# Kernel optimization log

Hardware: AMD Instinct MI355X
Metric: run time of the kernel (lower is better)

The kernel has to match this reference:

```python
import jax, jax.numpy as jnp
import numpy as np

D = 512; N = 1536; H = 4; DH = D // H
MAX_INT = 5; BINS = 100; LAYERS = 3


def _mha(q_in, k_in, v_in, in_w, in_b, out_w, out_b):
    """PyTorch-style nn.MultiheadAttention (batch of 1). Returns (out [Nq,D], head-avg weights [Nq,Nk])."""
    wq, wk, wv = in_w[:D], in_w[D:2 * D], in_w[2 * D:]
    bq, bk, bv = in_b[:D], in_b[D:2 * D], in_b[2 * D:]
    n_q, n_k = q_in.shape[0], k_in.shape[0]
    q = (q_in @ wq.T + bq).reshape(n_q, H, DH).transpose(1, 0, 2)  # [H,Nq,dh]
    k = (k_in @ wk.T + bk).reshape(n_k, H, DH).transpose(1, 0, 2)
    v = (v_in @ wv.T + bv).reshape(n_k, H, DH).transpose(1, 0, 2)
    scores = jnp.einsum('hqd,hkd->hqk', q, k) / jnp.sqrt(jnp.asarray(DH, q.dtype))
    w = jax.nn.softmax(scores, axis=-1)  # [H,Nq,Nk]
    out = jnp.einsum('hqk,hkd->hqd', w, v).transpose(1, 0, 2).reshape(n_q, D)
    out = out @ out_w.T + out_b
    return out, w.mean(0)


def setup_inputs() -> dict:
    key = jax.random.key(0)
    ks = jax.random.split(key, 12)
    s = 0.02
    return {
        'node_embeddings': jax.random.normal(ks[0], (N, D), jnp.float32),
        'time_positions': jax.random.uniform(ks[1], (N, 1), jnp.float32) * 10.0,
        'batch_indices': jnp.zeros((N,), jnp.int32),
        'W_time': jax.random.normal(ks[2], (D, 1), jnp.float32) * s,
        'b_time': jnp.zeros((D,), jnp.float32),
        'in_w': jax.random.normal(ks[3], (3 * D, D), jnp.float32) * s,
        'in_b': jnp.zeros((3 * D,), jnp.float32),
        'out_w': jax.random.normal(ks[4], (D, D), jnp.float32) * s,
        'out_b': jnp.zeros((D,), jnp.float32),
        'ic_w1': jax.random.normal(ks[5], (128, D), jnp.float32) * s,
        'ic_b1': jnp.zeros((128,), jnp.float32),
        'ic_w2': jax.random.normal(ks[6], (MAX_INT, 128), jnp.float32) * s,
        'ic_b2': jnp.zeros((MAX_INT,), jnp.float32),
        'ref_w1': jax.random.normal(ks[7], (LAYERS, 128, D + 2), jnp.float32) * s,
        'ref_b1': jnp.zeros((LAYERS, 128), jnp.float32),
        'ref_w2': jax.random.normal(ks[8], (LAYERS, 2 * BINS, 128), jnp.float32) * s,
        'ref_b2': jnp.zeros((LAYERS, 2 * BINS), jnp.float32),
        'weight_params': jnp.linspace(-0.5, 0.5, BINS).astype(jnp.float32),
        'qp_w': jax.random.normal(ks[9], (D, D + 2), jnp.float32) * s,
        'qp_b': jnp.zeros((D,), jnp.float32),
    }


def _forward(node_embeddings, time_positions, W_time, b_time, in_w, in_b, out_w, out_b,
             ic_w1, ic_b1, ic_w2, ic_b2, ref_w1, ref_b1, ref_w2, ref_b2,
             weight_params, qp_w, qp_b):
    x = node_embeddings + time_positions @ W_time.T + b_time  # [N,D]
    attn_out, _ = _mha(x, x, x, in_w, in_b, out_w, out_b)      # [N,D]
    pooled = attn_out.mean(0)                                   # [D]
    probs = jax.nn.softmax(ic_w2 @ jax.nn.relu(ic_w1 @ pooled + ic_b1) + ic_b2)
    num_intervals = jnp.argmax(probs) + 1
    interval_mask = jnp.arange(MAX_INT) < num_intervals
    t_min, t_max = time_positions.min(), time_positions.max()
    grid = jnp.linspace(t_min, t_max, MAX_INT + 1)
    start, end = grid[:-1], grid[1:]                            # [MAX_INT]
    n = attn_out.shape[0]
    ones = jnp.ones((n, 1), attn_out.dtype)

    def per_interval(s_i, e_i, w1, b1, w2, b2):
        query = jnp.concatenate([attn_out, ones * s_i, ones * e_i], axis=-1)  # [N,D+2]
        qp = query @ qp_w.T + qp_b                                            # [N,D]
        h = jax.nn.relu(query @ w1.T + b1)
        logits = h @ w2.T + b2                                                # [N,2*BINS]
        s_off = (jax.nn.softmax(logits[:, :BINS], axis=-1) * weight_params).sum(-1)  # [N]
        e_off = (jax.nn.softmax(logits[:, BINS:], axis=-1) * weight_params).sum(-1)
        _, aw = _mha(qp, attn_out, attn_out, in_w, in_b, out_w, out_b)        # [N,N]
        return (aw * s_off).sum(), (aw * e_off).sum()

    for l in range(LAYERS):  # layers have distinct params; intervals are independent within a layer
        ds, de = jax.vmap(per_interval, in_axes=(0, 0, None, None, None, None))(
            start, end, ref_w1[l], ref_b1[l], ref_w2[l], ref_b2[l])
        start = start + ds
        end = end + de

    final_bounds = jnp.stack([start, end], axis=-1)  # [MAX_INT,2]
    return final_bounds, interval_mask


def reference(node_embeddings, time_positions, batch_indices, W_time, b_time, in_w, in_b,
              out_w, out_b, ic_w1, ic_b1, ic_w2, ic_b2, ref_w1, ref_b1, ref_w2, ref_b2,
              weight_params, qp_w, qp_b):
    return _forward(node_embeddings, time_positions, W_time, b_time, in_w, in_b, out_w, out_b,
                    ic_w1, ic_b1, ic_w2, ic_b2, ref_w1, ref_b1, ref_w2, ref_b2,
                    weight_params, qp_w, qp_b)
```

## Files before the change

kernel.cpp:

```cpp
#include <hip/hip_runtime.h>
#include <hip/hip_bf16.h>

typedef __hip_bfloat16 bf16;
typedef __bf16 bf16x8 __attribute__((ext_vector_type(8)));
typedef float f32x4 __attribute__((ext_vector_type(4)));

#define DD   512
#define NT   1536
#define NH   4
#define DHD  128
#define NBINS 100
#define MAXI 5
#define NL   3
#define RSQRT_DH 0.08838834764831845f

#define OFF_X      ((size_t)0)
#define OFF_QKV    (OFF_X    + (size_t)NT*DD)
#define OFF_ATT    (OFF_QKV  + (size_t)NT*3*DD)
#define OFF_CTX    (OFF_ATT  + (size_t)NT*DD)
#define OFF_K2     (OFF_CTX  + (size_t)NT*DD)
#define OFF_QP0    (OFF_K2   + (size_t)NT*DD)
#define OFF_Q0     (OFF_QP0  + (size_t)NT*DD)
#define OFF_H0     (OFF_Q0   + (size_t)NT*DD)
#define OFF_HR     (OFF_H0   + (size_t)NT*384)
#define OFF_LG     (OFF_HR   + (size_t)MAXI*NT*128)
#define OFF_AARR   (OFF_LG   + (size_t)MAXI*NT*200)
#define OFF_BARR   (OFF_AARR + (size_t)NH*NT)
#define OFF_AV     (OFF_BARR + (size_t)NH*NT)
#define OFF_BV     (OFF_AV   + (size_t)DD)
#define OFF_SOFF   (OFF_BV   + (size_t)DD)
#define OFF_EOFF   (OFF_SOFF + (size_t)MAXI*NT)
#define OFF_RST    (OFF_EOFF + (size_t)MAXI*NT)
#define OFF_POOL   (OFF_RST  + (size_t)NH*NT*2)
#define OFF_SCAL   (OFF_POOL + (size_t)DD)
#define OFF_S      (OFF_SCAL + (size_t)64)
#define SC_START 0
#define SC_END   5
#define SC_DSDE  10
#define SC_CNT   20
#define OFF_QPT  (OFF_QP0)
#define OFF_M2   (OFF_QP0 + (size_t)512*512)
#define OFF_B2   (OFF_QP0 + (size_t)2*512*512)
#define PSLICE   ((size_t)NH*NT*16)

__global__ void k_pre(const float* __restrict__ t, float* ws) {
    __shared__ float smn[256], smx[256];
    int tid = threadIdx.x;
    ws[OFF_POOL + tid] = 0.f; ws[OFF_POOL + 256 + tid] = 0.f;
    float mn = 1e30f, mx = -1e30f;
    for (int i = tid; i < NT; i += 256) { float v = t[i]; mn = fminf(mn, v); mx = fmaxf(mx, v); }
    smn[tid] = mn; smx[tid] = mx; __syncthreads();
    for (int s = 128; s; s >>= 1) {
        if (tid < s) { smn[tid] = fminf(smn[tid], smn[tid + s]); smx[tid] = fmaxf(smx[tid], smx[tid + s]); }
        __syncthreads();
    }
    if (tid == 0) {
        float tmin = smn[0], tmax = smx[0];
        for (int i = 0; i < MAXI; i++) {
            ws[OFF_SCAL + SC_START + i] = tmin + (tmax - tmin) * (float)i / 5.0f;
            ws[OFF_SCAL + SC_END + i]   = tmin + (tmax - tmin) * (float)(i + 1) / 5.0f;
        }
    }
}

__global__ void k_qpt(const float* __restrict__ qp_w, float* ws) {
    __shared__ float tb[32][33];
    int c0 = blockIdx.x * 32, d0 = blockIdx.y * 32;
    int tid = threadIdx.x;
    int dd = tid >> 5, cc = tid & 31;
#pragma unroll
    for (int p = 0; p < 4; p++)
        tb[dd + p * 8][cc] = qp_w[(size_t)(d0 + dd + p * 8) * 514 + c0 + cc];
    __syncthreads();
    int cc2 = tid >> 5, dd2 = tid & 31;
    float* qpT = ws + OFF_QPT;
#pragma unroll
    for (int p = 0; p < 4; p++)
        qpT[(size_t)(c0 + cc2 + p * 8) * 512 + d0 + dd2] = tb[dd2][cc2 + p * 8];
}

template <int BF16OUT>
__global__ __launch_bounds__(256) void k_mgemm(
    const float* __restrict__ A, int lda, long long aZ,
    const float* __restrict__ B, int ldb, long long bZ,
    void* __restrict__ Cv, int ldc, long long cZ,
    int N, int K, float alpha, const float* __restrict__ bias)
{
    int z = blockIdx.z;
    A += (size_t)z * aZ; B += (size_t)z * bZ;
    int m0 = blockIdx.y * 128, n0 = blockIdx.x * 128;
    __shared__ __bf16 As[128 * 40];
    __shared__ __bf16 Bs[128 * 40];
    int tid = threadIdx.x;
    int r = tid >> 1, hh = tid & 1;
    int w = tid >> 6, lane = tid & 63;
    int wm = (w & 1) * 64, wn = (w >> 1) * 64;
    int lr = lane & 15, lq = lane >> 4;
    f32x4 acc[4][4];
#pragma unroll
    for (int i = 0; i < 4; i++)
#pragma unroll
        for (int j = 0; j < 4; j++) acc[i][j] = (f32x4){0.f, 0.f, 0.f, 0.f};

    int gnr = n0 + r;
    const float* arow = A + (size_t)(m0 + r) * lda + hh * 16;
    const float* brow = B + (size_t)gnr * ldb + hh * 16;
    __bf16* awr = &As[r * 40 + hh * 16];
    __bf16* bwr = &Bs[r * 40 + hh * 16];

    for (int k0 = 0; k0 < K; k0 += 32) {
        __bf16 ta[16] __attribute__((aligned(16)));
        __bf16 tb[16] __attribute__((aligned(16)));
#pragma unroll
        for (int q = 0; q < 8; q++) {
            float2 f = *(const float2*)(arow + k0 + 2 * q);
            ta[2 * q] = (__bf16)f.x; ta[2 * q + 1] = (__bf16)f.y;
        }
        if (gnr < N) {
#pragma unroll
            for (int q = 0; q < 8; q++) {
                float2 f = *(const float2*)(brow + k0 + 2 * q);
                tb[2 * q] = (__bf16)f.x; tb[2 * q + 1] = (__bf16)f.y;
            }
        } else {
#pragma unroll
            for (int q = 0; q < 16; q++) tb[q] = (__bf16)0.f;
        }
        __syncthreads();
        *(bf16x8*)awr = *(bf16x8*)ta;
        *(bf16x8*)(awr + 8) = *(bf16x8*)(ta + 8);
        *(bf16x8*)bwr = *(bf16x8*)tb;
        *(bf16x8*)(bwr + 8) = *(bf16x8*)(tb + 8);
        __syncthreads();
        bf16x8 af[4], bfr[4];
#pragma unroll
        for (int i = 0; i < 4; i++) af[i] = *(bf16x8*)&As[(wm + i * 16 + lr) * 40 + lq * 8];
#pragma unroll
        for (int j = 0; j < 4; j++) bfr[j] = *(bf16x8*)&Bs[(wn + j * 16 + lr) * 40 + lq * 8];
#pragma unroll
        for (int i = 0; i < 4; i++)
#pragma unroll
            for (int j = 0; j < 4; j++)
                acc[i][j] = __builtin_amdgcn_mfma_f32_16x16x32_bf16(af[i], bfr[j], acc[i][j], 0, 0, 0);
    }
#pragma unroll
    for (int i = 0; i < 4; i++) {
#pragma unroll
        for (int r4 = 0; r4 < 4; r4++) {
            int gm = m0 + wm + i * 16 + lq * 4 + r4;
#pragma unroll
            for (int j = 0; j < 4; j++) {
                int gn = n0 + wn + j * 16 + lr;
                if (gn < N) {
                    float v = acc[i][j][r4] * alpha + (bias ? bias[gn] : 0.f);
                    if (BF16OUT) ((bf16*)Cv)[cZ * z + (size_t)gm * ldc + gn] = __float2bfloat16(v);
                    else         ((float*)Cv)[cZ * z + (size_t)gm * ldc + gn] = v;
                }
            }
        }
    }
}

template <int BF16OUT>
__global__ __launch_bounds__(256) void k_g64(
    const float* __restrict__ A, int lda, long long aZ,
    const float* __restrict__ B, int ldb, long long bZ,
    void* __restrict__ Cv, int ldc, long long cZ,
    int N, int K, float alpha, const float* __restrict__ bias)
{
    int z = blockIdx.z;
    A += (size_t)z * aZ; B += (size_t)z * bZ;
    int m0 = blockIdx.y * 64, n0 = blockIdx.x * 64;
    __shared__ __bf16 As[64 * 40];
    __shared__ __bf16 Bs[64 * 40];
    int tid = threadIdx.x;
    int r = tid >> 2, quad = tid & 3;
    int w = tid >> 6, lane = tid & 63;
    int wm = (w & 1) * 32, wn = (w >> 1) * 32;
    int lr = lane & 15, lq = lane >> 4;
    f32x4 acc[2][2];
#pragma unroll
    for (int i = 0; i < 2; i++)
#pragma unroll
        for (int j = 0; j < 2; j++) acc[i][j] = (f32x4){0.f, 0.f, 0.f, 0.f};

    int gnr = n0 + r;
    const float* arow = A + (size_t)(m0 + r) * lda + quad * 8;
    const float* brow = B + (size_t)gnr * ldb + quad * 8;
    __bf16* awr = &As[r * 40 + quad * 8];
    __bf16* bwr = &Bs[r * 40 + quad * 8];

    for (int k0 = 0; k0 < K; k0 += 32) {
        __bf16 ta[8] __attribute__((aligned(16)));
        __bf16 tb[8] __attribute__((aligned(16)));
#pragma unroll
        for (int q = 0; q < 4; q++) {
            float2 f = *(const float2*)(arow + k0 + 2 * q);
            ta[2 * q] = (__bf16)f.x; ta[2 * q + 1] = (__bf16)f.y;
        }
        if (gnr < N) {
#pragma unroll
            for (int q = 0; q < 4; q++) {
                float2 f = *(const float2*)(brow + k0 + 2 * q);
                tb[2 * q] = (__bf16)f.x; tb[2 * q + 1] = (__bf16)f.y;
            }
        } else {
#pragma unroll
            for (int q = 0; q < 8; q++) tb[q] = (__bf16)0.f;
        }
        __syncthreads();
        *(bf16x8*)awr = *(bf16x8*)ta;
        *(bf16x8*)bwr = *(bf16x8*)tb;
        __syncthreads();
        bf16x8 af[2], bfr[2];
#pragma unroll
        for (int i = 0; i < 2; i++) af[i] = *(bf16x8*)&As[(wm + i * 16 + lr) * 40 + lq * 8];
#pragma unroll
        for (int j = 0; j < 2; j++) bfr[j] = *(bf16x8*)&Bs[(wn + j * 16 + lr) * 40 + lq * 8];
#pragma unroll
        for (int i = 0; i < 2; i++)
#pragma unroll
            for (int j = 0; j < 2; j++)
                acc[i][j] = __builtin_amdgcn_mfma_f32_16x16x32_bf16(af[i], bfr[j], acc[i][j], 0, 0, 0);
    }
#pragma unroll
    for (int i = 0; i < 2; i++) {
#pragma unroll
        for (int r4 = 0; r4 < 4; r4++) {
            int gm = m0 + wm + i * 16 + lq * 4 + r4;
#pragma unroll
            for (int j = 0; j < 2; j++) {
                int gn = n0 + wn + j * 16 + lr;
                if (gn < N) {
                    float v = acc[i][j][r4] * alpha + (bias ? bias[gn] : 0.f);
                    if (BF16OUT) ((bf16*)Cv)[cZ * z + (size_t)gm * ldc + gn] = __float2bfloat16(v);
                    else         ((float*)Cv)[cZ * z + (size_t)gm * ldc + gn] = v;
                }
            }
        }
    }
}

__global__ __launch_bounds__(256) void k_qkv(
    const float* __restrict__ emb, const float* __restrict__ t,
    const float* __restrict__ wt, const float* __restrict__ bt,
    const float* __restrict__ in_w, const float* __restrict__ in_b, float* ws)
{
    int m0 = blockIdx.y * 64, n0 = blockIdx.x * 64;
    __shared__ __bf16 As[64 * 40];
    __shared__ __bf16 Bs[64 * 40];
    int tid = threadIdx.x;
    int r = tid >> 2, quad = tid & 3;
    int w = tid >> 6, lane = tid & 63;
    int wm = (w & 1) * 32, wn = (w >> 1) * 32;
    int lr = lane & 15, lq = lane >> 4;
    f32x4 acc[2][2];
#pragma unroll
    for (int i = 0; i < 2; i++)
#pragma unroll
        for (int j = 0; j < 2; j++) acc[i][j] = (f32x4){0.f, 0.f, 0.f, 0.f};

    float trow = t[m0 + r];
    const float* arow = emb + (size_t)(m0 + r) * DD + quad * 8;
    const float* brow = in_w + (size_t)(n0 + r) * DD + quad * 8;
    __bf16* awr = &As[r * 40 + quad * 8];
    __bf16* bwr = &Bs[r * 40 + quad * 8];

    for (int k0 = 0; k0 < DD; k0 += 32) {
        __bf16 ta[8] __attribute__((aligned(16)));
        __bf16 tb[8] __attribute__((aligned(16)));
#pragma unroll
        for (int q = 0; q < 4; q++) {
            float2 e = *(const float2*)(arow + k0 + 2 * q);
            float2 wv = *(const float2*)(wt + k0 + quad * 8 + 2 * q);
            float2 bv = *(const float2*)(bt + k0 + quad * 8 + 2 * q);
            ta[2 * q]     = (__bf16)(e.x + trow * wv.x + bv.x);
            ta[2 * q + 1] = (__bf16)(e.y + trow * wv.y + bv.y);
            float2 f = *(const float2*)(brow + k0 + 2 * q);
            tb[2 * q] = (__bf16)f.x; tb[2 * q + 1] = (__bf16)f.y;
        }
        __syncthreads();
        *(bf16x8*)awr = *(bf16x8*)ta;
        *(bf16x8*)bwr = *(bf16x8*)tb;
        __syncthreads();
        bf16x8 af[2], bfr[2];
#pragma unroll
        for (int i = 0; i < 2; i++) af[i] = *(bf16x8*)&As[(wm + i * 16 + lr) * 40 + lq * 8];
#pragma unroll
        for (int j = 0; j < 2; j++) bfr[j] = *(bf16x8*)&Bs[(wn + j * 16 + lr) * 40 + lq * 8];
#pragma unroll
        for (int i = 0; i < 2; i++)
#pragma unroll
            for (int j = 0; j < 2; j++)
                acc[i][j] = __builtin_amdgcn_mfma_f32_16x16x32_bf16(af[i], bfr[j], acc[i][j], 0, 0, 0);
    }
    float* qkv = ws + OFF_QKV;
    float* Vt  = ws + OFF_X;
#pragma unroll
    for (int i = 0; i < 2; i++)
#pragma unroll
        for (int j = 0; j < 2; j++) {
            int gn = n0 + wn + j * 16 + lr;
            int gmb = m0 + wm + i * 16 + lq * 4;
            float b = in_b[gn];
            f32x4 vv = acc[i][j];
            vv[0] += b; vv[1] += b; vv[2] += b; vv[3] += b;
            if (gn < 2 * DD) {
#pragma unroll
                for (int r4 = 0; r4 < 4; r4++)
                    qkv[(size_t)(gmb + r4) * (3 * DD) + gn] = vv[r4];
            } else {
                *(float4*)&Vt[(size_t)(gn - 2 * DD) * NT + gmb] = *(float4*)&vv;
            }
        }
}

__global__ __launch_bounds__(256) void k_oproj(
    const float* __restrict__ out_w, const float* __restrict__ out_b, float* ws)
{
    int m0 = blockIdx.y * 64, n0 = blockIdx.x * 64;
    __shared__ __bf16 As[64 * 40];
    __shared__ __bf16 Bs[64 * 40];
    __shared__ float ps[64];
    int tid = threadIdx.x;
    int r = tid >> 2, quad = tid & 3;
    int w = tid >> 6, lane = tid & 63;
    int wm = (w & 1) * 32, wn = (w >> 1) * 32;
    int lr = lane & 15, lq = lane >> 4;
    f32x4 acc[2][2];
#pragma unroll
    for (int i = 0; i < 2; i++)
#pragma unroll
        for (int j = 0; j < 2; j++) acc[i][j] = (f32x4){0.f, 0.f, 0.f, 0.f};
    if (tid < 64) ps[tid] = 0.f;

    const float* a0 = ws + OFF_CTX + (size_t)(m0 + r) * DD + quad * 8;
    const float* a1 = ws + OFF_HR  + (size_t)(m0 + r) * DD + quad * 8;
    const float* brow = out_w + (size_t)(n0 + r) * DD + quad * 8;
    __bf16* awr = &As[r * 40 + quad * 8];
    __bf16* bwr = &Bs[r * 40 + quad * 8];

    for (int k0 = 0; k0 < DD; k0 += 32) {
        __bf16 ta[8] __attribute__((aligned(16)));
        __bf16 tb[8] __attribute__((aligned(16)));
#pragma unroll
        for (int q = 0; q < 4; q++) {
            float2 x = *(const float2*)(a0 + k0 + 2 * q);
            float2 y = *(const float2*)(a1 + k0 + 2 * q);
            ta[2 * q]     = (__bf16)(x.x + y.x);
            ta[2 * q + 1] = (__bf16)(x.y + y.y);
            float2 f = *(const float2*)(brow + k0 + 2 * q);
            tb[2 * q] = (__bf16)f.x; tb[2 * q + 1] = (__bf16)f.y;
        }
        __syncthreads();
        *(bf16x8*)awr = *(bf16x8*)ta;
        *(bf16x8*)bwr = *(bf16x8*)tb;
        __syncthreads();
        bf16x8 af[2], bfr[2];
#pragma unroll
        for (int i = 0; i < 2; i++) af[i] = *(bf16x8*)&As[(wm + i * 16 + lr) * 40 + lq * 8];
#pragma unroll
        for (int j = 0; j < 2; j++) bfr[j] = *(bf16x8*)&Bs[(wn + j * 16 + lr) * 40 + lq * 8];
#pragma unroll
        for (int i = 0; i < 2; i++)
#pragma unroll
            for (int j = 0; j < 2; j++)
                acc[i][j] = __builtin_amdgcn_mfma_f32_16x16x32_bf16(af[i], bfr[j], acc[i][j], 0, 0, 0);
    }
    float* att = ws + OFF_ATT;
#pragma unroll
    for (int j = 0; j < 2; j++) {
        int gn = n0 + wn + j * 16 + lr;
        float b = out_b[gn];
        float colsum = 0.f;
#pragma unroll
        for (int i = 0; i < 2; i++)
#pragma unroll
            for (int r4 = 0; r4 < 4; r4++) {
                int gm = m0 + wm + i * 16 + lq * 4 + r4;
                float v = acc[i][j][r4] + b;
                att[(size_t)gm * DD + gn] = v;
                colsum += v;
            }
        atomicAdd(&ps[wn + j * 16 + lr], colsum);
    }
    __syncthreads();
    if (tid < 64) atomicAdd(&ws[OFF_POOL + n0 + tid], ps[tid]);
}

__global__ __launch_bounds__(256) void k_trip(
    const float* __restrict__ in_w, const float* __restrict__ in_b,
    const float* __restrict__ ref_w1, const float* __restrict__ ref_b1, float* ws)
{
    int bx = blockIdx.x;
    const float* B; const float* bias; float* C; int ldb, ldc, n0;
    if (bx < 8)       { B = in_w + (size_t)DD * DD; ldb = DD;  bias = in_b + DD;   C = ws + OFF_K2; ldc = DD;  n0 = bx * 64; }
    else if (bx < 16) { B = ws + OFF_M2;            ldb = 512; bias = ws + OFF_B2; C = ws + OFF_Q0; ldc = DD;  n0 = (bx - 8) * 64; }
    else              { B = ref_w1;                 ldb = 514; bias = ref_b1;      C = ws + OFF_H0; ldc = 384; n0 = (bx - 16) * 64; }
    const float* A = ws + OFF_ATT;
    int m0 = blockIdx.y * 64;
    __shared__ __bf16 As[64 * 40];
    __shared__ __bf16 Bs[64 * 40];
    int tid = threadIdx.x;
    int r = tid >> 2, quad = tid & 3;
    int w = tid >> 6, lane = tid & 63;
    int wm = (w & 1) * 32, wn = (w >> 1) * 32;
    int lr = lane & 15, lq = lane >> 4;
    f32x4 acc[2][2];
#pragma unroll
    for (int i = 0; i < 2; i++)
#pragma unroll
        for (int j = 0; j < 2; j++) acc[i][j] = (f32x4){0.f, 0.f, 0.f, 0.f};

    const float* arow = A + (size_t)(m0 + r) * DD + quad * 8;
    const float* brow = B + (size_t)(n0 + r) * ldb + quad * 8;
    __bf16* awr = &As[r * 40 + quad * 8];
    __bf16* bwr = &Bs[r * 40 + quad * 8];

    for (int k0 = 0; k0 < DD; k0 += 32) {
        __bf16 ta[8] __attribute__((aligned(16)));
        __bf16 tb[8] __attribute__((aligned(16)));
#pragma unroll
        for (int q = 0; q < 4; q++) {
            float2 f = *(const float2*)(arow + k0 + 2 * q);
            ta[2 * q] = (__bf16)f.x; ta[2 * q + 1] = (__bf16)f.y;
            float2 g = *(const float2*)(brow + k0 + 2 * q);
            tb[2 * q] = (__bf16)g.x; tb[2 * q + 1] = (__bf16)g.y;
        }
        __syncthreads();
        *(bf16x8*)awr = *(bf16x8*)ta;
        *(bf16x8*)bwr = *(bf16x8*)tb;
        __syncthreads();
        bf16x8 af[2], bfr[2];
#pragma unroll
        for (int i = 0; i < 2; i++) af[i] = *(bf16x8*)&As[(wm + i * 16 + lr) * 40 + lq * 8];
#pragma unroll
        for (int j = 0; j < 2; j++) bfr[j] = *(bf16x8*)&Bs[(wn + j * 16 + lr) * 40 + lq * 8];
#pragma unroll
        for (int i = 0; i < 2; i++)
#pragma unroll
            for (int j = 0; j < 2; j++)
                acc[i][j] = __builtin_amdgcn_mfma_f32_16x16x32_bf16(af[i], bfr[j], acc[i][j], 0, 0, 0);
    }
#pragma unroll
    for (int i = 0; i < 2; i++)
#pragma unroll
        for (int r4 = 0; r4 < 4; r4++) {
            int gm = m0 + wm + i * 16 + lq * 4 + r4;
#pragma unroll
            for (int j = 0; j < 2; j++) {
                int gn = n0 + wn + j * 16 + lr;
                C[(size_t)gm * ldc + gn] = acc[i][j][r4] + bias[gn];
            }
        }
}

__global__ __launch_bounds__(256) void k_rstats(const bf16* __restrict__ S, float* ws) {
    int wave = threadIdx.x >> 6, lane = threadIdx.x & 63;
    int row = blockIdx.x * 4 + wave;
    const bf16* p = S + (size_t)row * NT;
    float v[24], m = -1e30f;
#pragma unroll
    for (int t = 0; t < 24; t++) { v[t] = __bfloat162float(p[t * 64 + lane]); m = fmaxf(m, v[t]); }
    for (int off = 32; off; off >>= 1) m = fmaxf(m, __shfl_xor(m, off));
    float s = 0.f;
#pragma unroll
    for (int t = 0; t < 24; t++) s += __expf(v[t] - m);
    for (int off = 32; off; off >>= 1) s += __shfl_xor(s, off);
    if (lane == 0) { ws[OFF_RST + 2 * row] = m; ws[OFF_RST + 2 * row + 1] = 1.f / s; }
}

__global__ __launch_bounds__(256) void k_rse(float* ws) {
    bf16* S = (bf16*)(ws + OFF_S);
    int wave = threadIdx.x >> 6, lane = threadIdx.x & 63;
    int row = blockIdx.x * 4 + wave;
    unsigned short* p = (unsigned short*)(S + (size_t)row * NT);
    union { uint4 u; unsigned short s[8]; } b[3];
    float v[24], m = -1e30f;
#pragma unroll
    for (int c = 0; c < 3; c++) {
        b[c].u = *(const uint4*)(p + c * 512 + lane * 8);
#pragma unroll
        for (int q = 0; q < 8; q++) {
            v[c * 8 + q] = __uint_as_float((unsigned)b[c].s[q] << 16);
            m = fmaxf(m, v[c * 8 + q]);
        }
    }
    for (int off = 32; off; off >>= 1) m = fmaxf(m, __shfl_xor(m, off));
#pragma unroll
    for (int c = 0; c < 3; c++) {
#pragma unroll
        for (int q = 0; q < 8; q++) {
            bf16 ov = __float2bfloat16(__expf(v[c * 8 + q] - m));
            b[c].s[q] = *(unsigned short*)&ov;
        }
        *(uint4*)(p + c * 512 + lane * 8) = b[c].u;
    }
}

__global__ __launch_bounds__(256) void k_pv(const bf16* __restrict__ S, float* ws) {
    int h = blockIdx.z;
    int m0 = blockIdx.y * 64;
    int n0 = (blockIdx.x & 1) * 64;
    int ks = blockIdx.x >> 1;
    const int KCH = NT / 2;
    int kbeg = ks * KCH;
    __shared__ __bf16 As[64 * 40];
    __shared__ __bf16 Bs[64 * 40];
    int tid = threadIdx.x;
    int r = tid >> 2, quad = tid & 3;
    int w = tid >> 6, lane = tid & 63;
    int wm = (w & 1) * 32, wn = (w >> 1) * 32;
    int lr = lane & 15, lq = lane >> 4;
    const float* rst = ws + OFF_RST;
    const float* Vt = ws + OFF_X + (size_t)h * DHD * NT;
    const bf16* Sh = S + (size_t)h * NT * NT;
    int row = m0 + r;
    float mrow = rst[2 * (h * NT + row)];
    const unsigned short* srow = (const unsigned short*)(Sh + (size_t)row * NT) + quad * 8;
    const float* brow = Vt + (size_t)(n0 + r) * NT + quad * 8;
    __bf16* awr = &As[r * 40 + quad * 8];
    __bf16* bwr = &Bs[r * 40 + quad * 8];
    f32x4 acc[2][2];
#pragma unroll
    for (int i = 0; i < 2; i++)
#pragma unroll
        for (int j = 0; j < 2; j++) acc[i][j] = (f32x4){0.f, 0.f, 0.f, 0.f};

    for (int k0 = kbeg; k0 < kbeg + KCH; k0 += 32) {
        union { uint4 u; unsigned short s[8]; } bb;
        bb.u = *(const uint4*)(srow + k0);
        __bf16 ta[8] __attribute__((aligned(16)));
        __bf16 tb[8] __attribute__((aligned(16)));
#pragma unroll
        for (int q = 0; q < 8; q++)
            ta[q] = (__bf16)__expf(__uint_as_float((unsigned)bb.s[q] << 16) - mrow);
#pragma unroll
        for (int q = 0; q < 4; q++) {
            float2 f = *(const float2*)(brow + k0 + 2 * q);
            tb[2 * q] = (__bf16)f.x; tb[2 * q + 1] = (__bf16)f.y;
        }
        __syncthreads();
        *(bf16x8*)awr = *(bf16x8*)ta;
        *(bf16x8*)bwr = *(bf16x8*)tb;
        __syncthreads();
        bf16x8 af[2], bfr[2];
#pragma unroll
        for (int i = 0; i < 2; i++) af[i] = *(bf16x8*)&As[(wm + i * 16 + lr) * 40 + lq * 8];
#pragma unroll
        for (int j = 0; j < 2; j++) bfr[j] = *(bf16x8*)&Bs[(wn + j * 16 + lr) * 40 + lq * 8];
#pragma unroll
        for (int i = 0; i < 2; i++)
#pragma unroll
            for (int j = 0; j < 2; j++)
                acc[i][j] = __builtin_amdgcn_mfma_f32_16x16x32_bf16(af[i], bfr[j], acc[i][j], 0, 0, 0);
    }
    float* dst = ws + (ks == 0 ? OFF_CTX : OFF_HR);
#pragma unroll
    for (int i = 0; i < 2; i++)
#pragma unroll
        for (int r4 = 0; r4 < 4; r4++) {
            int gm = m0 + wm + i * 16 + lq * 4 + r4;
            float ri = rst[2 * (h * NT + gm) + 1];
#pragma unroll
            for (int j = 0; j < 2; j++) {
                int gn = n0 + wn + j * 16 + lr;
                dst[(size_t)gm * DD + h * DHD + gn] = acc[i][j][r4] * ri;
            }
        }
}

__global__ void k_head(const float* __restrict__ icw1, const float* __restrict__ icb1,
                       const float* __restrict__ icw2, const float* __restrict__ icb2,
                       float* ws, float* out) {
    __shared__ float h1[128];
    __shared__ float lg[MAXI];
    int tid = threadIdx.x;
    float a = 0.f;
    for (int c = 0; c < DD; c++) a += icw1[(size_t)tid * DD + c] * ws[OFF_POOL + c];
    h1[tid] = fmaxf(a * (1.0f / NT) + icb1[tid], 0.f);
    __syncthreads();
    if (tid < MAXI) {
        float s = icb2[tid];
        for (int j = 0; j < 128; j++) s += icw2[tid * 128 + j] * h1[j];
        lg[tid] = s;
    }
    __syncthreads();
    if (tid == 0) {
        int best = 0; float bv = lg[0];
        for (int m = 1; m < MAXI; m++) if (lg[m] > bv) { bv = lg[m]; best = m; }
        int ni = best + 1;
        for (int i = 0; i < MAXI; i++) out[10 + i] = (i < ni) ? 1.f : 0.f;
    }
}

__global__ void k_uv(const float* __restrict__ in_w, const float* __restrict__ qp_w,
                     const float* __restrict__ qp_b, const float* __restrict__ in_b, float* ws) {
    __shared__ float su[DD], sv[DD], sb[DD];
    int tid = threadIdx.x;
    for (int c = tid; c < DD; c += 256) {
        su[c] = qp_w[c * 514 + 512]; sv[c] = qp_w[c * 514 + 513]; sb[c] = qp_b[c];
    }
    __syncthreads();
    int j = blockIdx.x * 256 + tid;
    float a = 0.f, b = 0.f, c2 = 0.f;
    for (int c = 0; c < DD; c++) {
        float w = in_w[(size_t)j * DD + c];
        a += w * su[c]; b += w * sv[c]; c2 += w * sb[c];
    }
    ws[OFF_AV + j] = a; ws[OFF_BV + j] = b; ws[OFF_B2 + j] = c2 + in_b[j];
}

__global__ __launch_bounds__(256) void k_ab(float* ws) {
    int wave = threadIdx.x >> 6, lane = threadIdx.x & 63;
    int row = blockIdx.x * 4 + wave;
    int h = row / NT, n = row % NT;
    const float* k2 = ws + OFF_K2 + (size_t)n * DD + h * DHD;
    const float* av = ws + OFF_AV + h * DHD;
    const float* bv = ws + OFF_BV + h * DHD;
    int d = lane * 2;
    float a = av[d] * k2[d] + av[d + 1] * k2[d + 1];
    float b = bv[d] * k2[d] + bv[d + 1] * k2[d + 1];
    for (int off = 32; off; off >>= 1) { a += __shfl_xor(a, off); b += __shfl_xor(b, off); }
    if (lane == 0) { ws[OFF_AARR + row] = a * RSQRT_DH; ws[OFF_BARR + row] = b * RSQRT_DH; }
}

__global__ __launch_bounds__(256) void k_lgs(
    const float* __restrict__ rw1, const float* __restrict__ rw2,
    const float* __restrict__ rb2, const float* __restrict__ wp, int l, float* ws)
{
    __shared__ float dsh[128];
    __shared__ __bf16 As[64 * 136];
    __shared__ __bf16 Bs[64 * 136];
    __shared__ __bf16 Ls[64 * 208];
    int tid = threadIdx.x;
    int m0 = blockIdx.x * 64;
    int i_int = m0 / NT;
    int nbase = m0 % NT;
    if (blockIdx.x == 0 && tid < 11) ws[OFF_SCAL + SC_DSDE + tid] = 0.f;
    if (tid < 128) {
        float s_i = ws[OFF_SCAL + SC_START + i_int], e_i = ws[OFF_SCAL + SC_END + i_int];
        const float* wr = rw1 + (size_t)(l * 128 + tid) * 514;
        dsh[tid] = s_i * wr[512] + e_i * wr[513];
    }
    __syncthreads();
    int r = tid >> 2, quad = tid & 3;
    {
        const float* arow = ws + OFF_H0 + (size_t)(nbase + r) * 384 + l * 128 + quad * 32;
        __bf16 tmp[32] __attribute__((aligned(16)));
#pragma unroll
        for (int q = 0; q < 16; q++) {
            float2 f = *(const float2*)(arow + 2 * q);
            int jj = quad * 32 + 2 * q;
            tmp[2 * q]     = (__bf16)fmaxf(f.x + dsh[jj], 0.f);
            tmp[2 * q + 1] = (__bf16)fmaxf(f.y + dsh[jj + 1], 0.f);
        }
        __bf16* aw = &As[r * 136 + quad * 32];
#pragma unroll
        for (int q = 0; q < 4; q++) *(bf16x8*)(aw + q * 8) = *(bf16x8*)(tmp + q * 8);
    }
    int w = tid >> 6, lane = tid & 63;
    int wm = (w & 1) * 32, wn = (w >> 1) * 32;
    int lr = lane & 15, lq = lane >> 4;
    for (int nt = 0; nt < 4; nt++) {
        int n0 = nt * 64;
        int gnr = n0 + r;
        __bf16 tmp[32] __attribute__((aligned(16)));
        if (gnr < 200) {
            const float* brow = rw2 + (size_t)gnr * 128 + quad * 32;
#pragma unroll
            for (int q = 0; q < 16; q++) {
                float2 f = *(const float2*)(brow + 2 * q);
                tmp[2 * q] = (__bf16)f.x; tmp[2 * q + 1] = (__bf16)f.y;
            }
        } else {
#pragma unroll
            for (int q = 0; q < 32; q++) tmp[q] = (__bf16)0.f;
        }
        __syncthreads();
        {
            __bf16* bw = &Bs[r * 136 + quad * 32];
#pragma unroll
            for (int q = 0; q < 4; q++) *(bf16x8*)(bw + q * 8) = *(bf16x8*)(tmp + q * 8);
        }
        __syncthreads();
        f32x4 acc[2][2];
#pragma unroll
        for (int i = 0; i < 2; i++)
#pragma unroll
            for (int j = 0; j < 2; j++) acc[i][j] = (f32x4){0.f, 0.f, 0.f, 0.f};
#pragma unroll
        for (int kk = 0; kk < 4; kk++) {
            bf16x8 af[2], bfr[2];
#pragma unroll
            for (int i = 0; i < 2; i++) af[i] = *(bf16x8*)&As[(wm + i * 16 + lr) * 136 + kk * 32 + lq * 8];
#pragma unroll
            for (int j = 0; j < 2; j++) bfr[j] = *(bf16x8*)&Bs[(wn + j * 16 + lr) * 136 + kk * 32 + lq * 8];
#pragma unroll
            for (int i = 0; i < 2; i++)
#pragma unroll
                for (int j = 0; j < 2; j++)
                    acc[i][j] = __builtin_amdgcn_mfma_f32_16x16x32_bf16(af[i], bfr[j], acc[i][j], 0, 0, 0);
        }
#pragma unroll
        for (int i = 0; i < 2; i++)
#pragma unroll
            for (int r4 = 0; r4 < 4; r4++) {
                int rl = wm + i * 16 + lq * 4 + r4;
#pragma unroll
                for (int j = 0; j < 2; j++) {
                    int gn = n0 + wn + j * 16 + lr;
                    if (gn < 200) Ls[rl * 208 + gn] = (__bf16)(acc[i][j][r4] + rb2[gn]);
                }
            }
    }
    __syncthreads();
    {
        int rloc = tid >> 2, q = tid & 3;
        int c0 = q * 50;
        const unsigned short* lrow = (const unsigned short*)&Ls[rloc * 208];
        float m = -1e30f;
#pragma unroll
        for (int c = 0; c < 50; c++)
            m = fmaxf(m, __uint_as_float((unsigned)lrow[c0 + c] << 16));
        m = fmaxf(m, __shfl_xor(m, 1));
        float den = 0.f, num = 0.f;
#pragma unroll
        for (int c = 0; c < 50; c++) {
            float p = __expf(__uint_as_float((unsigned)lrow[c0 + c] << 16) - m);
            den += p;
            int wc = c0 + c; if (wc >= NBINS) wc -= NBINS;
            num += p * wp[wc];
        }
        den += __shfl_xor(den, 1);
        num += __shfl_xor(num, 1);
        int n = nbase + rloc;
        if (q == 0)      ws[OFF_SOFF + (size_t)i_int * NT + n] = num / den;
        else if (q == 2) ws[OFF_EOFF + (size_t)i_int * NT + n] = num / den;
    }
}

__global__ __launch_bounds__(256) void k_eg(const bf16* __restrict__ E0, float* ws) {
    int h = blockIdx.z;
    int m0 = blockIdx.y * 128;
    int ks = blockIdx.x;
    const int KCH = NT / 8;
    __shared__ __bf16 As[128 * 40];
    __shared__ __bf16 Bs[16 * 40];
    int tid = threadIdx.x;
    int w = tid >> 6, lane = tid & 63;
    int lr = lane & 15, lq = lane >> 4;
    int r = tid >> 1, half = tid & 1;
    const bf16* Sh = E0 + (size_t)h * NT * NT;
    const unsigned short* arow = (const unsigned short*)(Sh + (size_t)(m0 + r) * NT) + half * 16;
    int wm = w * 32;
    f32x4 acc[2];
    acc[0] = (f32x4){0.f, 0.f, 0.f, 0.f};
    acc[1] = (f32x4){0.f, 0.f, 0.f, 0.f};
    int bc = tid >> 3, bk = tid & 7;
    int valid = (tid < 128) && (bc < 15);
    int ii = bc / 3, tt = bc - ii * 3;
    if (ii > 4) ii = 4;
    float s_i = 0.f, e_i = 0.f;
    if (valid) { s_i = ws[OFF_SCAL + SC_START + ii]; e_i = ws[OFF_SCAL + SC_END + ii]; }
    const float* Ar = ws + OFF_AARR + h * NT;
    const float* Br = ws + OFF_BARR + h * NT;
    const float* fo = ws + (tt == 2 ? OFF_EOFF : OFF_SOFF) + (size_t)ii * NT;

    for (int k0 = ks * KCH; k0 < ks * KCH + KCH; k0 += 32) {
        uint4 a0 = *(const uint4*)(arow + k0);
        uint4 a1 = *(const uint4*)(arow + k0 + 8);
        float bv[4] = {0.f, 0.f, 0.f, 0.f};
        if (valid) {
            float4 a4 = *(const float4*)(Ar + k0 + bk * 4);
            float4 b4 = *(const float4*)(Br + k0 + bk * 4);
            bv[0] = __expf(s_i * a4.x + e_i * b4.x);
            bv[1] = __expf(s_i * a4.y + e_i * b4.y);
            bv[2] = __expf(s_i * a4.z + e_i * b4.z);
            bv[3] = __expf(s_i * a4.w + e_i * b4.w);
            if (tt) {
                float4 f4 = *(const float4*)(fo + k0 + bk * 4);
                bv[0] *= f4.x; bv[1] *= f4.y; bv[2] *= f4.z; bv[3] *= f4.w;
            }
        }
        __syncthreads();
        *(uint4*)&As[r * 40 + half * 16] = a0;
        *(uint4*)&As[r * 40 + half * 16 + 8] = a1;
        if (tid < 128) {
            __bf16* bw = &Bs[bc * 40 + bk * 4];
            bw[0] = (__bf16)bv[0]; bw[1] = (__bf16)bv[1]; bw[2] = (__bf16)bv[2]; bw[3] = (__bf16)bv[3];
        }
        __syncthreads();
        bf16x8 bf0 = *(bf16x8*)&Bs[lr * 40 + lq * 8];
        bf16x8 af0 = *(bf16x8*)&As[(wm + lr) * 40 + lq * 8];
        bf16x8 af1 = *(bf16x8*)&As[(wm + 16 + lr) * 40 + lq * 8];
        acc[0] = __builtin_amdgcn_mfma_f32_16x16x32_bf16(af0, bf0, acc[0], 0, 0, 0);
        acc[1] = __builtin_amdgcn_mfma_f32_16x16x32_bf16(af1, bf0, acc[1], 0, 0, 0);
    }
    float* P = ws + OFF_LG + (size_t)ks * PSLICE;
    if (lr < 15) {
#pragma unroll
        for (int i = 0; i < 2; i++)
#pragma unroll
            for (int r4 = 0; r4 < 4; r4++) {
                int gm = m0 + wm + i * 16 + lq * 4 + r4;
                P[(size_t)(h * NT + gm) * 16 + lr] = acc[i][r4];
            }
    }
}

__global__ __launch_bounds__(256) void k_fin(float* ws) {
    __shared__ float part[4][10];
    int tid = threadIdx.x;
    int w = tid >> 6, lane = tid & 63;
    int row = blockIdx.x * 256 + tid;
    float acc[15];
#pragma unroll
    for (int c = 0; c < 15; c++) acc[c] = 0.f;
    for (int ks = 0; ks < 8; ks++) {
        const float* Pr = ws + OFF_LG + (size_t)ks * PSLICE + (size_t)row * 16;
#pragma unroll
        for (int c = 0; c < 15; c++) acc[c] += Pr[c];
    }
    float loc[10];
#pragma unroll
    for (int i = 0; i < MAXI; i++) {
        float den = acc[i * 3];
        loc[i]        = acc[i * 3 + 1] / den;
        loc[MAXI + i] = acc[i * 3 + 2] / den;
    }
#pragma unroll
    for (int c = 0; c < 10; c++)
        for (int off = 32; off; off >>= 1) loc[c] += __shfl_xor(loc[c], off);
    if (lane == 0) {
#pragma unroll
        for (int c = 0; c < 10; c++) part[w][c] = loc[c];
    }
    __syncthreads();
    if (tid < 10) {
        float s = part[0][tid] + part[1][tid] + part[2][tid] + part[3][tid];
        atomicAdd(&ws[OFF_SCAL + SC_DSDE + tid], s);
    }
    __threadfence();
    __syncthreads();
    if (tid == 0) {
        unsigned old = atomicAdd((unsigned*)&ws[OFF_SCAL + SC_CNT], 1u);
        if (old == 23) {
            for (int i = 0; i < MAXI; i++) {
                float ds = atomicAdd(&ws[OFF_SCAL + SC_DSDE + i], 0.f);
                float de = atomicAdd(&ws[OFF_SCAL + SC_DSDE + MAXI + i], 0.f);
                ws[OFF_SCAL + SC_START + i] += ds * 0.25f;
                ws[OFF_SCAL + SC_END + i]   += de * 0.25f;
            }
        }
    }
}

__global__ void k_final(const float* __restrict__ ws, float* out) {
    int tid = threadIdx.x;
    if (tid < MAXI) {
        out[2 * tid]     = ws[OFF_SCAL + SC_START + tid];
        out[2 * tid + 1] = ws[OFF_SCAL + SC_END + tid];
    }
}

extern "C" void kernel_launch(void* const* d_in, const int* in_sizes, int n_in,
                              void* d_out, int out_size, void* d_ws, size_t ws_size,
                              hipStream_t stream) {
    const float* emb    = (const float*)d_in[0];
    const float* tpos   = (const float*)d_in[1];
    const float* W_time = (const float*)d_in[3];
    const float* b_time = (const float*)d_in[4];
    const float* in_w   = (const float*)d_in[5];
    const float* in_b   = (const float*)d_in[6];
    const float* out_w  = (const float*)d_in[7];
    const float* out_b  = (const float*)d_in[8];
    const float* ic_w1  = (const float*)d_in[9];
    const float* ic_b1  = (const float*)d_in[10];
    const float* ic_w2  = (const float*)d_in[11];
    const float* ic_b2  = (const float*)d_in[12];
    const float* ref_w1 = (const float*)d_in[13];
    const float* ref_b1 = (const float*)d_in[14];
    const float* ref_w2 = (const float*)d_in[15];
    const float* ref_b2 = (const float*)d_in[16];
    const float* wp     = (const float*)d_in[17];
    const float* qp_w   = (const float*)d_in[18];
    const float* qp_b   = (const float*)d_in[19];
    float* ws  = (float*)d_ws;
    float* out = (float*)d_out;
    bf16* S = (bf16*)(ws + OFF_S);

    k_pre<<<1, 256, 0, stream>>>(tpos, ws);
    k_qpt<<<dim3(16, 16), 256, 0, stream>>>(qp_w, ws);
    k_g64<0><<<dim3(8, 8, 1), 256, 0, stream>>>(
        in_w, DD, 0, ws + OFF_QPT, 512, 0, ws + OFF_M2, 512, 0, 512, DD, 1.f, nullptr);
    k_uv<<<2, 256, 0, stream>>>(in_w, qp_w, qp_b, in_b, ws);

    k_qkv<<<dim3(24, 24), 256, 0, stream>>>(emb, tpos, W_time, b_time, in_w, in_b, ws);
    k_mgemm<1><<<dim3(12, 12, NH), 256, 0, stream>>>(
        ws + OFF_QKV, 3 * DD, DHD, ws + OFF_QKV + DD, 3 * DD, DHD,
        S, NT, (long long)NT * NT, NT, DHD, RSQRT_DH, nullptr);
    k_rstats<<<NH * NT / 4, 256, 0, stream>>>(S, ws);
    k_pv<<<dim3(4, NT / 64, NH), 256, 0, stream>>>(S, ws);
    k_oproj<<<dim3(8, 24), 256, 0, stream>>>(out_w, out_b, ws);
    k_head<<<1, 128, 0, stream>>>(ic_w1, ic_b1, ic_w2, ic_b2, ws, out);

    k_trip<<<dim3(22, 24), 256, 0, stream>>>(in_w, in_b, ref_w1, ref_b1, ws);
    k_ab<<<NH * NT / 4, 256, 0, stream>>>(ws);

    k_mgemm<1><<<dim3(12, 12, NH), 256, 0, stream>>>(
        ws + OFF_Q0, DD, DHD, ws + OFF_K2, DD, DHD,
        S, NT, (long long)NT * NT, NT, DHD, RSQRT_DH, nullptr);
    k_rse<<<NH * NT / 4, 256, 0, stream>>>(ws);

    for (int l = 0; l < NL; l++) {
        k_lgs<<<120, 256, 0, stream>>>(ref_w1, ref_w2 + (size_t)l * 200 * 128,
                                       ref_b2 + l * 200, wp, l, ws);
        k_eg<<<dim3(8, NT / 128, NH), 256, 0, stream>>>(S, ws);
        k_fin<<<NH * NT / 256, 256, 0, stream>>>(ws);
    }
    k_final<<<1, 32, 0, stream>>>(ws, out);
}
```

Baseline: 367.3 us.

## Fuse softmax row stats into score GEMM and merge small prep kernels

The score GEMM now emits per-tile row max and sum-of-exp partials, so the separate row-stats and row-stat-exp passes over the NxN score matrix are gone. The PV and evidence kernels recompute exp on the fly from the stored raw scores. Small setup kernels (min/max, transpose, qp GEMM, uv dot products) are merged into one multi-role launch, and the head and final-output kernels are folded into others. Launch count and full passes over the score matrix go down, in exchange for extra exp work inside the GEMM consumers.

```diff
diff --git a/kernel.cpp b/kernel.cpp
--- a/kernel.cpp
+++ b/kernel.cpp
@@ -38,59 +38,127 @@
 #define SC_END   5
 #define SC_DSDE  10
 #define SC_CNT   20
-#define OFF_QPT  (OFF_QP0)
 #define OFF_M2   (OFF_QP0 + (size_t)512*512)
 #define OFF_B2   (OFF_QP0 + (size_t)2*512*512)
 #define PSLICE   ((size_t)NH*NT*16)
-
-__global__ void k_pre(const float* __restrict__ t, float* ws) {
+#define OFF_STAT (OFF_LG + (size_t)8*PSLICE)
+
+__global__ __launch_bounds__(256) void k_misc(
+    const float* __restrict__ tpos, const float* __restrict__ in_w,
+    const float* __restrict__ in_b, const float* __restrict__ qp_w,
+    const float* __restrict__ qp_b, float* ws)
+{
+    __shared__ __bf16 As[64 * 40];
+    __shared__ __bf16 Bs[64 * 40];
     __shared__ float smn[256], smx[256];
-    int tid = threadIdx.x;
-    ws[OFF_POOL + tid] = 0.f; ws[OFF_POOL + 256 + tid] = 0.f;
-    float mn = 1e30f, mx = -1e30f;
-    for (int i = tid; i < NT; i += 256) { float v = t[i]; mn = fminf(mn, v); mx = fmaxf(mx, v); }
-    smn[tid] = mn; smx[tid] = mx; __syncthreads();
-    for (int s = 128; s; s >>= 1) {
-        if (tid < s) { smn[tid] = fminf(smn[tid], smn[tid + s]); smx[tid] = fmaxf(smx[tid], smx[tid + s]); }
-        __syncthreads();
-    }
-    if (tid == 0) {
-        float tmin = smn[0], tmax = smx[0];
-        for (int i = 0; i < MAXI; i++) {
-            ws[OFF_SCAL + SC_START + i] = tmin + (tmax - tmin) * (float)i / 5.0f;
-            ws[OFF_SCAL + SC_END + i]   = tmin + (tmax - tmin) * (float)(i + 1) / 5.0f;
-        }
-    }
-}
-
-__global__ void k_qpt(const float* __restrict__ qp_w, float* ws) {
-    __shared__ float tb[32][33];
-    int c0 = blockIdx.x * 32, d0 = blockIdx.y * 32;
-    int tid = threadIdx.x;
-    int dd = tid >> 5, cc = tid & 31;
-#pragma unroll
-    for (int p = 0; p < 4; p++)
-        tb[dd + p * 8][cc] = qp_w[(size_t)(d0 + dd + p * 8) * 514 + c0 + cc];
-    __syncthreads();
-    int cc2 = tid >> 5, dd2 = tid & 31;
-    float* qpT = ws + OFF_QPT;
-#pragma unroll
-    for (int p = 0; p < 4; p++)
-        qpT[(size_t)(c0 + cc2 + p * 8) * 512 + d0 + dd2] = tb[dd2][cc2 + p * 8];
-}
-
-template <int BF16OUT>
-__global__ __launch_bounds__(256) void k_mgemm(
+    int bx = blockIdx.x, tid = threadIdx.x;
+    if (bx < 64) {
+        int m0 = (bx >> 3) * 64, n0 = (bx & 7) * 64;
+        int r = tid >> 2, quad = tid & 3;
+        int w = tid >> 6, lane = tid & 63;
+        int wm = (w & 1) * 32, wn = (w >> 1) * 32;
+        int lr = lane & 15, lq = lane >> 4;
+        f32x4 acc[2][2];
+#pragma unroll
+        for (int i = 0; i < 2; i++)
+#pragma unroll
+            for (int j = 0; j < 2; j++) acc[i][j] = (f32x4){0.f, 0.f, 0.f, 0.f};
+        const float* arow = in_w + (size_t)(m0 + r) * DD + quad * 8;
+        int kk = tid >> 3, g = tid & 7;
+        for (int k0 = 0; k0 < DD; k0 += 32) {
+            __bf16 ta[8] __attribute__((aligned(16)));
+#pragma unroll
+            for (int q = 0; q < 4; q++) {
+                float2 f = *(const float2*)(arow + k0 + 2 * q);
+                ta[2 * q] = (__bf16)f.x; ta[2 * q + 1] = (__bf16)f.y;
+            }
+            const float* bsrc = qp_w + (size_t)(k0 + kk) * 514 + n0 + g * 8;
+            float4 b0 = *(const float4*)bsrc;
+            float4 b1 = *(const float4*)(bsrc + 4);
+            float bb[8] = {b0.x, b0.y, b0.z, b0.w, b1.x, b1.y, b1.z, b1.w};
+            __syncthreads();
+            *(bf16x8*)&As[r * 40 + quad * 8] = *(bf16x8*)ta;
+#pragma unroll
+            for (int q = 0; q < 8; q++) Bs[(g * 8 + q) * 40 + kk] = (__bf16)bb[q];
+            __syncthreads();
+            bf16x8 af[2], bfr[2];
+#pragma unroll
+            for (int i = 0; i < 2; i++) af[i] = *(bf16x8*)&As[(wm + i * 16 + lr) * 40 + lq * 8];
+#pragma unroll
+            for (int j = 0; j < 2; j++) bfr[j] = *(bf16x8*)&Bs[(wn + j * 16 + lr) * 40 + lq * 8];
+#pragma unroll
+            for (int i = 0; i < 2; i++)
+#pragma unroll
+                for (int j = 0; j < 2; j++)
+                    acc[i][j] = __builtin_amdgcn_mfma_f32_16x16x32_bf16(af[i], bfr[j], acc[i][j], 0, 0, 0);
+        }
+        float* M2 = ws + OFF_M2;
+#pragma unroll
+        for (int i = 0; i < 2; i++)
+#pragma unroll
+            for (int r4 = 0; r4 < 4; r4++) {
+                int gm = m0 + wm + i * 16 + lq * 4 + r4;
+#pragma unroll
+                for (int j = 0; j < 2; j++)
+                    M2[(size_t)gm * 512 + n0 + wn + j * 16 + lr] = acc[i][j][r4];
+            }
+    } else if (bx < 72) {
+        int w = tid >> 6, lane = tid & 63;
+        float su8[8], sv8[8], sb8[8];
+#pragma unroll
+        for (int q = 0; q < 8; q++) {
+            int c = lane * 8 + q;
+            su8[q] = qp_w[(size_t)c * 514 + 512];
+            sv8[q] = qp_w[(size_t)c * 514 + 513];
+            sb8[q] = qp_b[c];
+        }
+        int base = (bx - 64) * 64 + w * 16;
+        for (int t = 0; t < 16; t++) {
+            int row = base + t;
+            const float* wr = in_w + (size_t)row * DD + lane * 8;
+            float4 x0 = *(const float4*)wr, x1 = *(const float4*)(wr + 4);
+            float xa[8] = {x0.x, x0.y, x0.z, x0.w, x1.x, x1.y, x1.z, x1.w};
+            float a = 0.f, b = 0.f, c2 = 0.f;
+#pragma unroll
+            for (int q = 0; q < 8; q++) { a += xa[q] * su8[q]; b += xa[q] * sv8[q]; c2 += xa[q] * sb8[q]; }
+            for (int off = 32; off; off >>= 1) {
+                a += __shfl_xor(a, off); b += __shfl_xor(b, off); c2 += __shfl_xor(c2, off);
+            }
+            if (lane == 0) {
+                ws[OFF_AV + row] = a; ws[OFF_BV + row] = b; ws[OFF_B2 + row] = c2 + in_b[row];
+            }
+        }
+    } else {
+        ws[OFF_POOL + tid] = 0.f; ws[OFF_POOL + 256 + tid] = 0.f;
+        float mn = 1e30f, mx = -1e30f;
+        for (int i = tid; i < NT; i += 256) { float v = tpos[i]; mn = fminf(mn, v); mx = fmaxf(mx, v); }
+        smn[tid] = mn; smx[tid] = mx; __syncthreads();
+        for (int s = 128; s; s >>= 1) {
+            if (tid < s) { smn[tid] = fminf(smn[tid], smn[tid + s]); smx[tid] = fmaxf(smx[tid], smx[tid + s]); }
+            __syncthreads();
+        }
+        if (tid == 0) {
+            float tmin = smn[0], tmax = smx[0];
+            for (int i = 0; i < MAXI; i++) {
+                ws[OFF_SCAL + SC_START + i] = tmin + (tmax - tmin) * (float)i / 5.0f;
+                ws[OFF_SCAL + SC_END + i]   = tmin + (tmax - tmin) * (float)(i + 1) / 5.0f;
+            }
+        }
+    }
+}
+
+__global__ __launch_bounds__(256) void k_score(
     const float* __restrict__ A, int lda, long long aZ,
     const float* __restrict__ B, int ldb, long long bZ,
-    void* __restrict__ Cv, int ldc, long long cZ,
-    int N, int K, float alpha, const float* __restrict__ bias)
+    bf16* __restrict__ C, float* __restrict__ stat)
 {
     int z = blockIdx.z;
     A += (size_t)z * aZ; B += (size_t)z * bZ;
     int m0 = blockIdx.y * 128, n0 = blockIdx.x * 128;
     __shared__ __bf16 As[128 * 40];
     __shared__ __bf16 Bs[128 * 40];
+    __shared__ float sMax[4][64];
+    __shared__ float sSum[4][64];
     int tid = threadIdx.x;
     int r = tid >> 1, hh = tid & 1;
     int w = tid >> 6, lane = tid & 63;
@@ -102,29 +170,20 @@
 #pragma unroll
         for (int j = 0; j < 4; j++) acc[i][j] = (f32x4){0.f, 0.f, 0.f, 0.f};
 
-    int gnr = n0 + r;
     const float* arow = A + (size_t)(m0 + r) * lda + hh * 16;
-    const float* brow = B + (size_t)gnr * ldb + hh * 16;
+    const float* brow = B + (size_t)(n0 + r) * ldb + hh * 16;
     __bf16* awr = &As[r * 40 + hh * 16];
     __bf16* bwr = &Bs[r * 40 + hh * 16];
 
-    for (int k0 = 0; k0 < K; k0 += 32) {
+    for (int k0 = 0; k0 < DHD; k0 += 32) {
         __bf16 ta[16] __attribute__((aligned(16)));
         __bf16 tb[16] __attribute__((aligned(16)));
 #pragma unroll
         for (int q = 0; q < 8; q++) {
             float2 f = *(const float2*)(arow + k0 + 2 * q);
             ta[2 * q] = (__bf16)f.x; ta[2 * q + 1] = (__bf16)f.y;
-        }
-        if (gnr < N) {
-#pragma unroll
-            for (int q = 0; q < 8; q++) {
-                float2 f = *(const float2*)(brow + k0 + 2 * q);
-                tb[2 * q] = (__bf16)f.x; tb[2 * q + 1] = (__bf16)f.y;
-            }
-        } else {
-#pragma unroll
-            for (int q = 0; q < 16; q++) tb[q] = (__bf16)0.f;
+            float2 g = *(const float2*)(brow + k0 + 2 * q);
+            tb[2 * q] = (__bf16)g.x; tb[2 * q + 1] = (__bf16)g.y;
         }
         __syncthreads();
         *(bf16x8*)awr = *(bf16x8*)ta;
@@ -144,100 +203,47 @@
                 acc[i][j] = __builtin_amdgcn_mfma_f32_16x16x32_bf16(af[i], bfr[j], acc[i][j], 0, 0, 0);
     }
 #pragma unroll
-    for (int i = 0; i < 4; i++) {
+    for (int i = 0; i < 4; i++)
 #pragma unroll
         for (int r4 = 0; r4 < 4; r4++) {
             int gm = m0 + wm + i * 16 + lq * 4 + r4;
 #pragma unroll
             for (int j = 0; j < 4; j++) {
                 int gn = n0 + wn + j * 16 + lr;
-                if (gn < N) {
-                    float v = acc[i][j][r4] * alpha + (bias ? bias[gn] : 0.f);
-                    if (BF16OUT) ((bf16*)Cv)[cZ * z + (size_t)gm * ldc + gn] = __float2bfloat16(v);
-                    else         ((float*)Cv)[cZ * z + (size_t)gm * ldc + gn] = v;
-                }
-            }
-        }
-    }
-}
-
-template <int BF16OUT>
-__global__ __launch_bounds__(256) void k_g64(
-    const float* __restrict__ A, int lda, long long aZ,
-    const float* __restrict__ B, int ldb, long long bZ,
-    void* __restrict__ Cv, int ldc, long long cZ,
-    int N, int K, float alpha, const float* __restrict__ bias)
-{
-    int z = blockIdx.z;
-    A += (size_t)z * aZ; B += (size_t)z * bZ;
-    int m0 = blockIdx.y * 64, n0 = blockIdx.x * 64;
-    __shared__ __bf16 As[64 * 40];
-    __shared__ __bf16 Bs[64 * 40];
-    int tid = threadIdx.x;
-    int r = tid >> 2, quad = tid & 3;
-    int w = tid >> 6, lane = tid & 63;
-    int wm = (w & 1) * 32, wn = (w >> 1) * 32;
-    int lr = lane & 15, lq = lane >> 4;
-    f32x4 acc[2][2];
-#pragma unroll
-    for (int i = 0; i < 2; i++)
-#pragma unroll
-        for (int j = 0; j < 2; j++) acc[i][j] = (f32x4){0.f, 0.f, 0.f, 0.f};
-
-    int gnr = n0 + r;
-    const float* arow = A + (size_t)(m0 + r) * lda + quad * 8;
-    const float* brow = B + (size_t)gnr * ldb + quad * 8;
-    __bf16* awr = &As[r * 40 + quad * 8];
-    __bf16* bwr = &Bs[r * 40 + quad * 8];
-
-    for (int k0 = 0; k0 < K; k0 += 32) {
-        __bf16 ta[8] __attribute__((aligned(16)));
-        __bf16 tb[8] __attribute__((aligned(16)));
-#pragma unroll
-        for (int q = 0; q < 4; q++) {
-            float2 f = *(const float2*)(arow + k0 + 2 * q);
-            ta[2 * q] = (__bf16)f.x; ta[2 * q + 1] = (__bf16)f.y;
-        }
-        if (gnr < N) {
-#pragma unroll
-            for (int q = 0; q < 4; q++) {
-                float2 f = *(const float2*)(brow + k0 + 2 * q);
-                tb[2 * q] = (__bf16)f.x; tb[2 * q + 1] = (__bf16)f.y;
-            }
-        } else {
-#pragma unroll
-            for (int q = 0; q < 8; q++) tb[q] = (__bf16)0.f;
-        }
-        __syncthreads();
-        *(bf16x8*)awr = *(bf16x8*)ta;
-        *(bf16x8*)bwr = *(bf16x8*)tb;
-        __syncthreads();
-        bf16x8 af[2], bfr[2];
-#pragma unroll
-        for (int i = 0; i < 2; i++) af[i] = *(bf16x8*)&As[(wm + i * 16 + lr) * 40 + lq * 8];
-#pragma unroll
-        for (int j = 0; j < 2; j++) bfr[j] = *(bf16x8*)&Bs[(wn + j * 16 + lr) * 40 + lq * 8];
-#pragma unroll
-        for (int i = 0; i < 2; i++)
-#pragma unroll
-            for (int j = 0; j < 2; j++)
-                acc[i][j] = __builtin_amdgcn_mfma_f32_16x16x32_bf16(af[i], bfr[j], acc[i][j], 0, 0, 0);
-    }
-#pragma unroll
-    for (int i = 0; i < 2; i++) {
+                C[(size_t)z * NT * NT + (size_t)gm * NT + gn] =
+                    __float2bfloat16(acc[i][j][r4] * RSQRT_DH);
+            }
+        }
+#pragma unroll
+    for (int i = 0; i < 4; i++)
 #pragma unroll
         for (int r4 = 0; r4 < 4; r4++) {
-            int gm = m0 + wm + i * 16 + lq * 4 + r4;
-#pragma unroll
-            for (int j = 0; j < 2; j++) {
-                int gn = n0 + wn + j * 16 + lr;
-                if (gn < N) {
-                    float v = acc[i][j][r4] * alpha + (bias ? bias[gn] : 0.f);
-                    if (BF16OUT) ((bf16*)Cv)[cZ * z + (size_t)gm * ldc + gn] = __float2bfloat16(v);
-                    else         ((float*)Cv)[cZ * z + (size_t)gm * ldc + gn] = v;
-                }
-            }
-        }
+            float m = -1e30f;
+#pragma unroll
+            for (int j = 0; j < 4; j++) m = fmaxf(m, acc[i][j][r4] * RSQRT_DH);
+            for (int off = 1; off < 16; off <<= 1) m = fmaxf(m, __shfl_xor(m, off));
+            if (lr == 0) sMax[w][i * 16 + lq * 4 + r4] = m;
+        }
+    __syncthreads();
+#pragma unroll
+    for (int i = 0; i < 4; i++)
+#pragma unroll
+        for (int r4 = 0; r4 < 4; r4++) {
+            int lidx = i * 16 + lq * 4 + r4;
+            float M = fmaxf(sMax[w][lidx], sMax[w ^ 2][lidx]);
+            float s = 0.f;
+#pragma unroll
+            for (int j = 0; j < 4; j++) s += __expf(acc[i][j][r4] * RSQRT_DH - M);
+            for (int off = 1; off < 16; off <<= 1) s += __shfl_xor(s, off);
+            if (lr == 0) sSum[w][lidx] = s;
+        }
+    __syncthreads();
+    if (tid < 128) {
+        int lidx = tid & 63, wb = tid >> 6;
+        float M = fmaxf(sMax[wb][lidx], sMax[wb + 2][lidx]);
+        float den = sSum[wb][lidx] + sSum[wb + 2][lidx];
+        size_t base = ((size_t)z * NT + m0 + tid) * 24 + (size_t)blockIdx.x * 2;
+        stat[base] = M; stat[base + 1] = den;
     }
 }
 
@@ -315,6 +321,88 @@
         }
 }
 
+__global__ __launch_bounds__(256) void k_pv(const bf16* __restrict__ S, float* ws) {
+    int h = blockIdx.z;
+    int m0 = blockIdx.y * 64;
+    int n0 = (blockIdx.x & 1) * 64;
+    int ks = blockIdx.x >> 1;
+    const int KCH = NT / 2;
+    int kbeg = ks * KCH;
+    __shared__ __bf16 As[64 * 40];
+    __shared__ __bf16 Bs[64 * 40];
+    __shared__ float sM[64], sI[64];
+    int tid = threadIdx.x;
+    if (tid < 64) {
+        const float* st = ws + OFF_STAT + ((size_t)(h * NT + m0 + tid)) * 24;
+        float M = -1e30f;
+#pragma unroll
+        for (int t2 = 0; t2 < 12; t2++) M = fmaxf(M, st[2 * t2]);
+        float den = 0.f;
+#pragma unroll
+        for (int t2 = 0; t2 < 12; t2++) den += st[2 * t2 + 1] * __expf(st[2 * t2] - M);
+        sM[tid] = M; sI[tid] = 1.f / den;
+    }
+    __syncthreads();
+    int r = tid >> 2, quad = tid & 3;
+    int w = tid >> 6, lane = tid & 63;
+    int wm = (w & 1) * 32, wn = (w >> 1) * 32;
+    int lr = lane & 15, lq = lane >> 4;
+    const float* Vt = ws + OFF_X + (size_t)h * DHD * NT;
+    const bf16* Sh = S + (size_t)h * NT * NT;
+    float mrow = sM[r];
+    const unsigned short* srow = (const unsigned short*)(Sh + (size_t)(m0 + r) * NT) + quad * 8;
+    const float* brow = Vt + (size_t)(n0 + r) * NT + quad * 8;
+    __bf16* awr = &As[r * 40 + quad * 8];
+    __bf16* bwr = &Bs[r * 40 + quad * 8];
+    f32x4 acc[2][2];
+#pragma unroll
+    for (int i = 0; i < 2; i++)
+#pragma unroll
+        for (int j = 0; j < 2; j++) acc[i][j] = (f32x4){0.f, 0.f, 0.f, 0.f};
+
+    for (int k0 = kbeg; k0 < kbeg + KCH; k0 += 32) {
+        union { uint4 u; unsigned short s[8]; } bb;
+        bb.u = *(const uint4*)(srow + k0);
+        __bf16 ta[8] __attribute__((aligned(16)));
+        __bf16 tb[8] __attribute__((aligned(16)));
+#pragma unroll
+        for (int q = 0; q < 8; q++)
+            ta[q] = (__bf16)__expf(__uint_as_float((unsigned)bb.s[q] << 16) - mrow);
+#pragma unroll
+        for (int q = 0; q < 4; q++) {
+            float2 f = *(const float2*)(brow + k0 + 2 * q);
+            tb[2 * q] = (__bf16)f.x; tb[2 * q + 1] = (__bf16)f.y;
+        }
+        __syncthreads();
+        *(bf16x8*)awr = *(bf16x8*)ta;
+        *(bf16x8*)bwr = *(bf16x8*)tb;
+        __syncthreads();
+        bf16x8 af[2], bfr[2];
+#pragma unroll
+        for (int i = 0; i < 2; i++) af[i] = *(bf16x8*)&As[(wm + i * 16 + lr) * 40 + lq * 8];
+#pragma unroll
+        for (int j = 0; j < 2; j++) bfr[j] = *(bf16x8*)&Bs[(wn + j * 16 + lr) * 40 + lq * 8];
+#pragma unroll
+        for (int i = 0; i < 2; i++)
+#pragma unroll
+            for (int j = 0; j < 2; j++)
+                acc[i][j] = __builtin_amdgcn_mfma_f32_16x16x32_bf16(af[i], bfr[j], acc[i][j], 0, 0, 0);
+    }
+    float* dst = ws + (ks == 0 ? OFF_CTX : OFF_HR);
+#pragma unroll
+    for (int i = 0; i < 2; i++)
+#pragma unroll
+        for (int r4 = 0; r4 < 4; r4++) {
+            int lrow = wm + i * 16 + lq * 4 + r4;
+            float ri = sI[lrow];
+#pragma unroll
+            for (int j = 0; j < 2; j++) {
+                int gn = n0 + wn + j * 16 + lr;
+                dst[(size_t)(m0 + lrow) * DD + h * DHD + gn] = acc[i][j][r4] * ri;
+            }
+        }
+}
+
 __global__ __launch_bounds__(256) void k_oproj(
     const float* __restrict__ out_w, const float* __restrict__ out_b, float* ws)
 {
@@ -390,18 +478,52 @@
 
 __global__ __launch_bounds__(256) void k_trip(
     const float* __restrict__ in_w, const float* __restrict__ in_b,
-    const float* __restrict__ ref_w1, const float* __restrict__ ref_b1, float* ws)
+    const float* __restrict__ ref_w1, const float* __restrict__ ref_b1,
+    const float* __restrict__ icw1, const float* __restrict__ icb1,
+    const float* __restrict__ icw2, const float* __restrict__ icb2,
+    float* ws, float* out)
 {
-    int bx = blockIdx.x;
+    __shared__ __bf16 As[64 * 40];
+    __shared__ __bf16 Bs[64 * 40];
+    __shared__ float h1[128];
+    __shared__ float lg[MAXI];
+    int bx = blockIdx.x, tid = threadIdx.x;
+    if (bx == 22) {
+        if (blockIdx.y != 0) return;
+        int w = tid >> 6, lane = tid & 63;
+        const float* pp = ws + OFF_POOL + lane * 8;
+        float4 p0 = *(const float4*)pp, p1 = *(const float4*)(pp + 4);
+        float p8[8] = {p0.x, p0.y, p0.z, p0.w, p1.x, p1.y, p1.z, p1.w};
+        for (int t = 0; t < 32; t++) {
+            int row = w * 32 + t;
+            const float* wr = icw1 + (size_t)row * DD + lane * 8;
+            float4 a = *(const float4*)wr, b = *(const float4*)(wr + 4);
+            float d = a.x * p8[0] + a.y * p8[1] + a.z * p8[2] + a.w * p8[3]
+                    + b.x * p8[4] + b.y * p8[5] + b.z * p8[6] + b.w * p8[7];
+            for (int off = 32; off; off >>= 1) d += __shfl_xor(d, off);
+            if (lane == 0) h1[row] = fmaxf(d * (1.0f / NT) + icb1[row], 0.f);
+        }
+        __syncthreads();
+        if (tid < MAXI) {
+            float s = icb2[tid];
+            for (int j = 0; j < 128; j++) s += icw2[tid * 128 + j] * h1[j];
+            lg[tid] = s;
+        }
+        __syncthreads();
+        if (tid == 0) {
+            int best = 0; float bv = lg[0];
+            for (int m = 1; m < MAXI; m++) if (lg[m] > bv) { bv = lg[m]; best = m; }
+            int ni = best + 1;
+            for (int i = 0; i < MAXI; i++) out[10 + i] = (i < ni) ? 1.f : 0.f;
+        }
+        return;
+    }
     const float* B; const float* bias; float* C; int ldb, ldc, n0;
     if (bx < 8)       { B = in_w + (size_t)DD * DD; ldb = DD;  bias = in_b + DD;   C = ws + OFF_K2; ldc = DD;  n0 = bx * 64; }
     else if (bx < 16) { B = ws + OFF_M2;            ldb = 512; bias = ws + OFF_B2; C = ws + OFF_Q0; ldc = DD;  n0 = (bx - 8) * 64; }
     else              { B = ref_w1;                 ldb = 514; bias = ref_b1;      C = ws + OFF_H0; ldc = 384; n0 = (bx - 16) * 64; }
     const float* A = ws + OFF_ATT;
     int m0 = blockIdx.y * 64;
-    __shared__ __bf16 As[64 * 40];
-    __shared__ __bf16 Bs[64 * 40];
-    int tid = threadIdx.x;
     int r = tid >> 2, quad = tid & 3;
     int w = tid >> 6, lane = tid & 63;
     int wm = (w & 1) * 32, wn = (w >> 1) * 32;
@@ -455,163 +577,7 @@
         }
 }
 
-__global__ __launch_bounds__(256) void k_rstats(const bf16* __restrict__ S, float* ws) {
-    int wave = threadIdx.x >> 6, lane = threadIdx.x & 63;
-    int row = blockIdx.x * 4 + wave;
-    const bf16* p = S + (size_t)row * NT;
-    float v[24], m = -1e30f;
-#pragma unroll
-    for (int t = 0; t < 24; t++) { v[t] = __bfloat162float(p[t * 64 + lane]); m = fmaxf(m, v[t]); }
-    for (int off = 32; off; off >>= 1) m = fmaxf(m, __shfl_xor(m, off));
-    float s = 0.f;
-#pragma unroll
-    for (int t = 0; t < 24; t++) s += __expf(v[t] - m);
-    for (int off = 32; off; off >>= 1) s += __shfl_xor(s, off);
-    if (lane == 0) { ws[OFF_RST + 2 * row] = m; ws[OFF_RST + 2 * row + 1] = 1.f / s; }
-}
-
-__global__ __launch_bounds__(256) void k_rse(float* ws) {
-    bf16* S = (bf16*)(ws + OFF_S);
-    int wave = threadIdx.x >> 6, lane = threadIdx.x & 63;
-    int row = blockIdx.x * 4 + wave;
-    unsigned short* p = (unsigned short*)(S + (size_t)row * NT);
-    union { uint4 u; unsigned short s[8]; } b[3];
-    float v[24], m = -1e30f;
-#pragma unroll
-    for (int c = 0; c < 3; c++) {
-        b[c].u = *(const uint4*)(p + c * 512 + lane * 8);
-#pragma unroll
-        for (int q = 0; q < 8; q++) {
-            v[c * 8 + q] = __uint_as_float((unsigned)b[c].s[q] << 16);
-            m = fmaxf(m, v[c * 8 + q]);
-        }
-    }
-    for (int off = 32; off; off >>= 1) m = fmaxf(m, __shfl_xor(m, off));
-#pragma unroll
-    for (int c = 0; c < 3; c++) {
-#pragma unroll
-        for (int q = 0; q < 8; q++) {
-            bf16 ov = __float2bfloat16(__expf(v[c * 8 + q] - m));
-            b[c].s[q] = *(unsigned short*)&ov;
-        }
-        *(uint4*)(p + c * 512 + lane * 8) = b[c].u;
-    }
-}
-
-__global__ __launch_bounds__(256) void k_pv(const bf16* __restrict__ S, float* ws) {
-    int h = blockIdx.z;
-    int m0 = blockIdx.y * 64;
-    int n0 = (blockIdx.x & 1) * 64;
-    int ks = blockIdx.x >> 1;
-    const int KCH = NT / 2;
-    int kbeg = ks * KCH;
-    __shared__ __bf16 As[64 * 40];
-    __shared__ __bf16 Bs[64 * 40];
-    int tid = threadIdx.x;
-    int r = tid >> 2, quad = tid & 3;
-    int w = tid >> 6, lane = tid & 63;
-    int wm = (w & 1) * 32, wn = (w >> 1) * 32;
-    int lr = lane & 15, lq = lane >> 4;
-    const float* rst = ws + OFF_RST;
-    const float* Vt = ws + OFF_X + (size_t)h * DHD * NT;
-    const bf16* Sh = S + (size_t)h * NT * NT;
-    int row = m0 + r;
-    float mrow = rst[2 * (h * NT + row)];
-    const unsigned short* srow = (const unsigned short*)(Sh + (size_t)row * NT) + quad * 8;
-    const float* brow = Vt + (size_t)(n0 + r) * NT + quad * 8;
-    __bf16* awr = &As[r * 40 + quad * 8];
-    __bf16* bwr = &Bs[r * 40 + quad * 8];
-    f32x4 acc[2][2];
-#pragma unroll
-    for (int i = 0; i < 2; i++)
-#pragma unroll
-        for (int j = 0; j < 2; j++) acc[i][j] = (f32x4){0.f, 0.f, 0.f, 0.f};
-
-    for (int k0 = kbeg; k0 < kbeg + KCH; k0 += 32) {
-        union { uint4 u; unsigned short s[8]; } bb;
-        bb.u = *(const uint4*)(srow + k0);
-        __bf16 ta[8] __attribute__((aligned(16)));
-        __bf16 tb[8] __attribute__((aligned(16)));
-#pragma unroll
-        for (int q = 0; q < 8; q++)
-            ta[q] = (__bf16)__expf(__uint_as_float((unsigned)bb.s[q] << 16) - mrow);
-#pragma unroll
-        for (int q = 0; q < 4; q++) {
-            float2 f = *(const float2*)(brow + k0 + 2 * q);
-            tb[2 * q] = (__bf16)f.x; tb[2 * q + 1] = (__bf16)f.y;
-        }
-        __syncthreads();
-        *(bf16x8*)awr = *(bf16x8*)ta;
-        *(bf16x8*)bwr = *(bf16x8*)tb;
-        __syncthreads();
-        bf16x8 af[2], bfr[2];
-#pragma unroll
-        for (int i = 0; i < 2; i++) af[i] = *(bf16x8*)&As[(wm + i * 16 + lr) * 40 + lq * 8];
-#pragma unroll
-        for (int j = 0; j < 2; j++) bfr[j] = *(bf16x8*)&Bs[(wn + j * 16 + lr) * 40 + lq * 8];
-#pragma unroll
-        for (int i = 0; i < 2; i++)
-#pragma unroll
-            for (int j = 0; j < 2; j++)
-                acc[i][j] = __builtin_amdgcn_mfma_f32_16x16x32_bf16(af[i], bfr[j], acc[i][j], 0, 0, 0);
-    }
-    float* dst = ws + (ks == 0 ? OFF_CTX : OFF_HR);
-#pragma unroll
-    for (int i = 0; i < 2; i++)
-#pragma unroll
-        for (int r4 = 0; r4 < 4; r4++) {
-            int gm = m0 + wm + i * 16 + lq * 4 + r4;
-            float ri = rst[2 * (h * NT + gm) + 1];
-#pragma unroll
-            for (int j = 0; j < 2; j++) {
-                int gn = n0 + wn + j * 16 + lr;
-                dst[(size_t)gm * DD + h * DHD + gn] = acc[i][j][r4] * ri;
-            }
-        }
-}
-
-__global__ void k_head(const float* __restrict__ icw1, const float* __restrict__ icb1,
-                       const float* __restrict__ icw2, const float* __restrict__ icb2,
-                       float* ws, float* out) {
-    __shared__ float h1[128];
-    __shared__ float lg[MAXI];
-    int tid = threadIdx.x;
-    float a = 0.f;
-    for (int c = 0; c < DD; c++) a += icw1[(size_t)tid * DD + c] * ws[OFF_POOL + c];
-    h1[tid] = fmaxf(a * (1.0f / NT) + icb1[tid], 0.f);
-    __syncthreads();
-    if (tid < MAXI) {
-        float s = icb2[tid];
-        for (int j = 0; j < 128; j++) s += icw2[tid * 128 + j] * h1[j];
-        lg[tid] = s;
-    }
-    __syncthreads();
-    if (tid == 0) {
-        int best = 0; float bv = lg[0];
-        for (int m = 1; m < MAXI; m++) if (lg[m] > bv) { bv = lg[m]; best = m; }
-        int ni = best + 1;
-        for (int i = 0; i < MAXI; i++) out[10 + i] = (i < ni) ? 1.f : 0.f;
-    }
-}
-
-__global__ void k_uv(const float* __restrict__ in_w, const float* __restrict__ qp_w,
-                     const float* __restrict__ qp_b, const float* __restrict__ in_b, float* ws) {
-    __shared__ float su[DD], sv[DD], sb[DD];
-    int tid = threadIdx.x;
-    for (int c = tid; c < DD; c += 256) {
-        su[c] = qp_w[c * 514 + 512]; sv[c] = qp_w[c * 514 + 513]; sb[c] = qp_b[c];
-    }
-    __syncthreads();
-    int j = blockIdx.x * 256 + tid;
-    float a = 0.f, b = 0.f, c2 = 0.f;
-    for (int c = 0; c < DD; c++) {
-        float w = in_w[(size_t)j * DD + c];
-        a += w * su[c]; b += w * sv[c]; c2 += w * sb[c];
-    }
-    ws[OFF_AV + j] = a; ws[OFF_BV + j] = b; ws[OFF_B2 + j] = c2 + in_b[j];
-}
-
-__global__ __launch_bounds__(256) void k_ab(float* ws) {
+__global__ __launch_bounds__(256) void k_abc(float* ws) {
     int wave = threadIdx.x >> 6, lane = threadIdx.x & 63;
     int row = blockIdx.x * 4 + wave;
     int h = row / NT, n = row % NT;
@@ -621,8 +587,14 @@
     int d = lane * 2;
     float a = av[d] * k2[d] + av[d + 1] * k2[d + 1];
     float b = bv[d] * k2[d] + bv[d + 1] * k2[d + 1];
+    float tm = (lane < 12) ? ws[OFF_STAT + (size_t)row * 24 + lane * 2] : -1e30f;
     for (int off = 32; off; off >>= 1) { a += __shfl_xor(a, off); b += __shfl_xor(b, off); }
-    if (lane == 0) { ws[OFF_AARR + row] = a * RSQRT_DH; ws[OFF_BARR + row] = b * RSQRT_DH; }
+    for (int off = 1; off < 16; off <<= 1) tm = fmaxf(tm, __shfl_xor(tm, off));
+    if (lane == 0) {
+        ws[OFF_AARR + row] = a * RSQRT_DH;
+        ws[OFF_BARR + row] = b * RSQRT_DH;
+        ws[OFF_RST + row] = tm;
+    }
 }
 
 __global__ __launch_bounds__(256) void k_lgs(
@@ -740,7 +712,7 @@
     }
 }
 
-__global__ __launch_bounds__(256) void k_eg(const bf16* __restrict__ E0, float* ws) {
+__global__ __launch_bounds__(256) void k_eg(const bf16* __restrict__ S0, float* ws) {
     int h = blockIdx.z;
     int m0 = blockIdx.y * 128;
     int ks = blockIdx.x;
@@ -751,8 +723,9 @@
     int w = tid >> 6, lane = tid & 63;
     int lr = lane & 15, lq = lane >> 4;
     int r = tid >> 1, half = tid & 1;
-    const bf16* Sh = E0 + (size_t)h * NT * NT;
+    const bf16* Sh = S0 + (size_t)h * NT * NT;
     const unsigned short* arow = (const unsigned short*)(Sh + (size_t)(m0 + r) * NT) + half * 16;
+    float mrow = ws[OFF_RST + h * NT + m0 + r];
     int wm = w * 32;
     f32x4 acc[2];
     acc[0] = (f32x4){0.f, 0.f, 0.f, 0.f};
@@ -768,8 +741,16 @@
     const float* fo = ws + (tt == 2 ? OFF_EOFF : OFF_SOFF) + (size_t)ii * NT;
 
     for (int k0 = ks * KCH; k0 < ks * KCH + KCH; k0 += 32) {
-        uint4 a0 = *(const uint4*)(arow + k0);
-        uint4 a1 = *(const uint4*)(arow + k0 + 8);
+        union { uint4 u; unsigned short s[8]; } a0, a1, o0, o1;
+        a0.u = *(const uint4*)(arow + k0);
+        a1.u = *(const uint4*)(arow + k0 + 8);
+#pragma unroll
+        for (int q = 0; q < 8; q++) {
+            __bf16 e0 = (__bf16)__expf(__uint_as_float((unsigned)a0.s[q] << 16) - mrow);
+            __bf16 e1 = (__bf16)__expf(__uint_as_float((unsigned)a1.s[q] << 16) - mrow);
+            o0.s[q] = *(unsigned short*)&e0;
+            o1.s[q] = *(unsigned short*)&e1;
+        }
         float bv[4] = {0.f, 0.f, 0.f, 0.f};
         if (valid) {
             float4 a4 = *(const float4*)(Ar + k0 + bk * 4);
@@ -784,8 +765,8 @@
             }
         }
         __syncthreads();
-        *(uint4*)&As[r * 40 + half * 16] = a0;
-        *(uint4*)&As[r * 40 + half * 16 + 8] = a1;
+        *(uint4*)&As[r * 40 + half * 16] = o0.u;
+        *(uint4*)&As[r * 40 + half * 16 + 8] = o1.u;
         if (tid < 128) {
             __bf16* bw = &Bs[bc * 40 + bk * 4];
             bw[0] = (__bf16)bv[0]; bw[1] = (__bf16)bv[1]; bw[2] = (__bf16)bv[2]; bw[3] = (__bf16)bv[3];
@@ -809,7 +790,7 @@
     }
 }
 
-__global__ __launch_bounds__(256) void k_fin(float* ws) {
+__global__ __launch_bounds__(256) void k_fin(float* ws, float* out, int l) {
     __shared__ float part[4][10];
     int tid = threadIdx.x;
     int w = tid >> 6, lane = tid & 63;
@@ -849,18 +830,13 @@
             for (int i = 0; i < MAXI; i++) {
                 float ds = atomicAdd(&ws[OFF_SCAL + SC_DSDE + i], 0.f);
                 float de = atomicAdd(&ws[OFF_SCAL + SC_DSDE + MAXI + i], 0.f);
-                ws[OFF_SCAL + SC_START + i] += ds * 0.25f;
-                ws[OFF_SCAL + SC_END + i]   += de * 0.25f;
-            }
-        }
-    }
-}
-
-__global__ void k_final(const float* __restrict__ ws, float* out) {
-    int tid = threadIdx.x;
-    if (tid < MAXI) {
-        out[2 * tid]     = ws[OFF_SCAL + SC_START + tid];
-        out[2 * tid + 1] = ws[OFF_SCAL + SC_END + tid];
+                float ns = ws[OFF_SCAL + SC_START + i] + ds * 0.25f;
+                float ne = ws[OFF_SCAL + SC_END + i]   + de * 0.25f;
+                ws[OFF_SCAL + SC_START + i] = ns;
+                ws[OFF_SCAL + SC_END + i]   = ne;
+                if (l == NL - 1) { out[2 * i] = ns; out[2 * i + 1] = ne; }
+            }
+        }
     }
 }
 
@@ -890,34 +866,25 @@
     float* out = (float*)d_out;
     bf16* S = (bf16*)(ws + OFF_S);
 
-    k_pre<<<1, 256, 0, stream>>>(tpos, ws);
-    k_qpt<<<dim3(16, 16), 256, 0, stream>>>(qp_w, ws);
-    k_g64<0><<<dim3(8, 8, 1), 256, 0, stream>>>(
-        in_w, DD, 0, ws + OFF_QPT, 512, 0, ws + OFF_M2, 512, 0, 512, DD, 1.f, nullptr);
-    k_uv<<<2, 256, 0, stream>>>(in_w, qp_w, qp_b, in_b, ws);
+    k_misc<<<73, 256, 0, stream>>>(tpos, in_w, in_b, qp_w, qp_b, ws);
 
     k_qkv<<<dim3(24, 24), 256, 0, stream>>>(emb, tpos, W_time, b_time, in_w, in_b, ws);
-    k_mgemm<1><<<dim3(12, 12, NH), 256, 0, stream>>>(
-        ws + OFF_QKV, 3 * DD, DHD, ws + OFF_QKV + DD, 3 * DD, DHD,
-        S, NT, (long long)NT * NT, NT, DHD, RSQRT_DH, nullptr);
-    k_rstats<<<NH * NT / 4, 256, 0, stream>>>(S, ws);
+    k_score<<<dim3(12, 12, NH), 256, 0, stream>>>(
+        ws + OFF_QKV, 3 * DD, DHD, ws + OFF_QKV + DD, 3 * DD, DHD, S, ws + OFF_STAT);
     k_pv<<<dim3(4, NT / 64, NH), 256, 0, stream>>>(S, ws);
     k_oproj<<<dim3(8, 24), 256, 0, stream>>>(out_w, out_b, ws);
-    k_head<<<1, 128, 0, stream>>>(ic_w1, ic_b1, ic_w2, ic_b2, ws, out);
-
-    k_trip<<<dim3(22, 24), 256, 0, stream>>>(in_w, in_b, ref_w1, ref_b1, ws);
-    k_ab<<<NH * NT / 4, 256, 0, stream>>>(ws);
-
-    k_mgemm<1><<<dim3(12, 12, NH), 256, 0, stream>>>(
-        ws + OFF_Q0, DD, DHD, ws + OFF_K2, DD, DHD,
-        S, NT, (long long)NT * NT, NT, DHD, RSQRT_DH, nullptr);
-    k_rse<<<NH * NT / 4, 256, 0, stream>>>(ws);
+
+    k_trip<<<dim3(23, 24), 256, 0, stream>>>(in_w, in_b, ref_w1, ref_b1,
+                                             ic_w1, ic_b1, ic_w2, ic_b2, ws, out);
+
+    k_score<<<dim3(12, 12, NH), 256, 0, stream>>>(
+        ws + OFF_Q0, DD, DHD, ws + OFF_K2, DD, DHD, S, ws + OFF_STAT);
+    k_abc<<<NH * NT / 4, 256, 0, stream>>>(ws);
 
     for (int l = 0; l < NL; l++) {
         k_lgs<<<120, 256, 0, stream>>>(ref_w1, ref_w2 + (size_t)l * 200 * 128,
                                        ref_b2 + l * 200, wp, l, ws);
         k_eg<<<dim3(8, NT / 128, NH), 256, 0, stream>>>(S, ws);
-        k_fin<<<NH * NT / 256, 256, 0, stream>>>(ws);
-    }
-    k_final<<<1, 32, 0, stream>>>(ws, out);
-}
+        k_fin<<<NH * NT / 256, 256, 0, stream>>>(ws, out, l);
+    }
+}
```

New measurement: 357.9 us. 1.03x faster.
